# Kernel optimization log

Measured on AMD Instinct MI355X. Metric: run time of the kernel, lower is better.

Reference implementation:

```python
import jax, jax.numpy as jnp
import numpy as np

B, C, H, W = 2, 192, 64, 64
NHEADS = 8


def setup_inputs() -> dict:
    key = jax.random.key(0)
    ks = jax.random.split(key, 6)
    L = H * W
    return {
        "x": jax.random.normal(ks[0], (B, C, H, W), dtype=jnp.float32),
        "mask": jax.random.normal(ks[1], (B, L, L), dtype=jnp.float32),
        "w_qkv": jax.random.normal(ks[2], (3 * C, C), dtype=jnp.float32) * (1.0 / np.sqrt(C)),
        "b_qkv": jax.random.normal(ks[3], (3 * C,), dtype=jnp.float32) * 0.02,
        "w_proj": jax.random.normal(ks[4], (C, C), dtype=jnp.float32) * (1.0 / np.sqrt(C)),
        "b_proj": jax.random.normal(ks[5], (C,), dtype=jnp.float32) * 0.02,
        "num_heads": NHEADS,
    }


def reference(x, mask, w_qkv, b_qkv, w_proj, b_proj, num_heads):
    b, c, h, w = x.shape
    L = h * w
    hd = c // num_heads  # head dim
    # 1x1 conv == per-pixel linear over channels
    qkv = jnp.einsum('bchw,oc->bohw', x, w_qkv) + b_qkv[None, :, None, None]
    q, k, v = jnp.split(qkv, 3, axis=1)  # each [b, c, h, w]

    def to_heads(t):
        # b (head hd) h w -> b head (h w) hd
        return t.reshape(b, num_heads, hd, L).transpose(0, 1, 3, 2)

    q, k, v = to_heads(q), to_heads(k), to_heads(v)
    scale = num_heads ** (-0.5)  # NOTE: original scales by num_heads, not head_dim
    attn = jnp.einsum('bnld,bnmd->bnlm', q, k) * scale + mask[:, None, :, :]
    attn = jax.nn.softmax(attn, axis=-1)
    out = jnp.einsum('bnlm,bnmd->bnld', attn, v)  # [b, head, L, hd]
    # b head L hd -> b (head hd) h w
    out = out.transpose(0, 1, 3, 2).reshape(b, c, h, w)
    out = jnp.einsum('bchw,oc->bohw', out, w_proj) + b_proj[None, :, None, None]
    return out
```

## Files before the change

### kernel.cpp

```cpp
#include <hip/hip_runtime.h>

#define B_  2
#define C_  192
#define L_  4096
#define NH_ 8
#define HD_ 24
#define C3_ 576
#define KV_ 64
#define NSPL_ 4
#define LSPL_ (L_ / NSPL_)
#define NTS_ (LSPL_ / KV_)
#define HG_ 4
#define KSTR_ 20

typedef _Float16 f16;
typedef __attribute__((ext_vector_type(8))) f16 f16x8;
typedef __attribute__((ext_vector_type(16))) float f32x16;

#define L2E_ 1.4426950408889634f

__device__ __forceinline__ int pk2(float a, float b) {
    union { __fp16 h __attribute__((ext_vector_type(2))); int i; } u;
    u.h = __builtin_amdgcn_cvt_pkrtz(a, b);
    return u.i;
}
__device__ __forceinline__ int pk2_rte(float a, float b) {
    union { f16 h[2]; int i; } u;
    u.h[0] = (f16)a; u.h[1] = (f16)b;
    return u.i;
}
__device__ __forceinline__ float ex2(float x) {
    float r;
    asm("v_exp_f32 %0, %1" : "=v"(r) : "v"(x));
    return r;
}
__device__ __forceinline__ float lg2(float x) {
    float r;
    asm("v_log_f32 %0, %1" : "=v"(r) : "v"(x));
    return r;
}

union Frag { f16x8 v; int i[4]; };

#define MFMA32(A, Bx, Cc) __builtin_amdgcn_mfma_f32_32x32x16_f16((A), (Bx), (Cc), 0, 0, 0)

__device__ __forceinline__ void gload4(const void* g, void* lds) {
    typedef const unsigned int __attribute__((address_space(1))) as1u;
    typedef unsigned int __attribute__((address_space(3))) as3u;
    __builtin_amdgcn_global_load_lds((as1u*)g,
                                     (as3u*)(unsigned int)(unsigned long long)lds,
                                     4, 0, 0);
}
__device__ __forceinline__ void gload16(const void* g, void* lds) {
    typedef const unsigned int __attribute__((address_space(1))) as1u;
    typedef unsigned int __attribute__((address_space(3))) as3u;
    __builtin_amdgcn_global_load_lds((as1u*)g,
                                     (as3u*)(unsigned int)(unsigned long long)lds,
                                     16, 0, 0);
}

__global__ __launch_bounds__(256) void lin_qkv(const float* __restrict__ a,
                                               const float* __restrict__ w,
                                               const float* __restrict__ bias,
                                               unsigned int* __restrict__ q2,
                                               unsigned int* __restrict__ k2t,
                                               unsigned short* __restrict__ v16) {
    __shared__ float wl[8][C_];
    const int og  = blockIdx.x;
    const int b   = blockIdx.y >> 4;
    const int lt  = blockIdx.y & 15;
    const int tid = threadIdx.x;

    for (int e = tid; e < 8 * C_; e += 256) wl[e / C_][e % C_] = w[og * 8 * C_ + e];
    __syncthreads();

    const int l = lt * 256 + tid;
    float acc[8];
#pragma unroll
    for (int j = 0; j < 8; ++j) acc[j] = bias[og * 8 + j];

    const float* ap = a + (size_t)b * C_ * L_ + l;
#pragma unroll 2
    for (int c = 0; c < C_; ++c) {
        const float xv = ap[(size_t)c * L_];
#pragma unroll
        for (int j = 0; j < 8; ++j) acc[j] = fmaf(wl[j][c], xv, acc[j]);
    }

    const float qscale = 0.35355339059327373f * L2E_;
    if (og < 24) {
        const int h = og / 3, j0 = (og % 3) * 4;
        unsigned int* p = q2 + ((size_t)(b * NH_ + h) * 12 + j0) * L_ + l;
#pragma unroll
        for (int j = 0; j < 4; ++j)
            p[(size_t)j * L_] = pk2_rte(acc[2 * j] * qscale, acc[2 * j + 1] * qscale);
    } else if (og < 48) {
        const int og_ = og - 24;
        const int h = og_ / 3, j0 = (og_ % 3) * 4;
        unsigned int* p = k2t + ((size_t)(b * NH_ + h) * L_ + l) * KSTR_ + j0;
        int4 v;
        v.x = pk2_rte(acc[0], acc[1]); v.y = pk2_rte(acc[2], acc[3]);
        v.z = pk2_rte(acc[4], acc[5]); v.w = pk2_rte(acc[6], acc[7]);
        *(int4*)p = v;
        if (j0 == 8) {
            int4 z; z.x = z.y = z.z = z.w = 0;
            *(int4*)(p + 4) = z;
            *(int4*)(p + 8) = z;
        }
    } else {
        const int og_ = og - 48;
        const int h = og_ / 3, d0 = (og_ % 3) * 8;
        unsigned short* p = v16 + ((size_t)(b * NH_ + h) * 24 + d0) * L_ + l;
#pragma unroll
        for (int j = 0; j < 8; ++j) {
            union { f16 hf; unsigned short us; } cv;
            cv.hf = (f16)acc[j];
            p[(size_t)j * L_] = cv.us;
        }
    }
}

__global__ __launch_bounds__(256) void lin_kernel(const float* __restrict__ a,
                                                  const float* __restrict__ w,
                                                  const float* __restrict__ bias,
                                                  float* __restrict__ out, int OC) {
    __shared__ float wl[8][C_];
    const int og  = blockIdx.x;
    const int b   = blockIdx.y >> 4;
    const int lt  = blockIdx.y & 15;
    const int tid = threadIdx.x;

    for (int e = tid; e < 8 * C_; e += 256) wl[e / C_][e % C_] = w[og * 8 * C_ + e];
    __syncthreads();

    const int l = lt * 256 + tid;
    float acc[8];
#pragma unroll
    for (int j = 0; j < 8; ++j) acc[j] = bias[og * 8 + j];

    const float* ap = a + (size_t)b * C_ * L_ + l;
#pragma unroll 2
    for (int c = 0; c < C_; ++c) {
        const float xv = ap[(size_t)c * L_];
#pragma unroll
        for (int j = 0; j < 8; ++j) acc[j] = fmaf(wl[j][c], xv, acc[j]);
    }

    float* op = out + ((size_t)b * OC + og * 8) * L_ + l;
#pragma unroll
    for (int j = 0; j < 8; ++j) op[(size_t)j * L_] = acc[j];
}

__global__ __launch_bounds__(256) void attn_mfma(const unsigned int* __restrict__ q2,
                                                 const unsigned int* __restrict__ k2t,
                                                 const unsigned short* __restrict__ v16,
                                                 const float* __restrict__ mask,
                                                 unsigned short* __restrict__ po,
                                                 float* __restrict__ pms) {
    const int tid  = threadIdx.x;
    const int lane = tid & 63;
    const int wid  = tid >> 6;
    const int hi   = lane >> 5;
    const int lq   = lane & 31;
    const int bid  = blockIdx.x;
    const int qt   = bid & 31;
    const int r    = bid >> 5;
    const int b    = r & 1;
    const int hg   = (r >> 1) & 1;
    const int sp   = r >> 2;
    const int qrow = qt * 128 + wid * 32 + lq;
    const int kv0  = sp * LSPL_;
    const int hbase = hg * HG_;

    __shared__ __attribute__((aligned(16))) int k_lds[2][HG_][64 * KSTR_];
    __shared__ __attribute__((aligned(16))) int v_lds[2][HG_][32 * 32];

    const unsigned int*   qb   = q2  + (size_t)(b * NH_ + hbase) * 12 * L_;
    const unsigned int*   kb_w = k2t + (size_t)(b * NH_ + hbase + wid) * L_ * KSTR_;
    const unsigned short* vb_w = v16 + (size_t)(b * NH_ + hbase + wid) * 24 * L_;
    const float* mrow = mask + ((size_t)b * L_ + qrow) * L_;

    int bq[HG_][8];
#pragma unroll
    for (int H = 0; H < HG_; ++H)
#pragma unroll
        for (int s = 0; s < 2; ++s)
#pragma unroll
            for (int t = 0; t < 4; ++t) {
                const int dpq = 8 * s + 4 * hi + t;
                bq[H][s * 4 + t] = (dpq < 12) ? qb[(size_t)(H * 12 + dpq) * L_ + qrow] : 0;
            }

#define STAGE(BF, KK) do {                                                    \
    const char* ksrc_ = (const char*)kb_w + (size_t)(KK) * 80 + (size_t)lane * 16; \
    char* kdst_ = (char*)&k_lds[BF][wid][0];                                  \
    _Pragma("unroll")                                                         \
    for (int j_ = 0; j_ < 5; ++j_)                                            \
        gload16(ksrc_ + j_ * 1024, kdst_ + j_ * 1024);                        \
    _Pragma("unroll")                                                         \
    for (int j_ = 0; j_ < 12; ++j_) {                                         \
        const int d_ = j_ * 2 + (lane >> 5);                                  \
        const int c_ = lane & 31;                                             \
        const int kp_ = ((((c_ >> 2) ^ (d_ & 7)) << 2) | (c_ & 3));           \
        gload4(vb_w + (size_t)d_ * L_ + (KK) + 2 * kp_,                       \
               (char*)&v_lds[BF][wid][0] + j_ * 256);                         \
    } } while (0)

#define MLOADX(KK) do {                                                       \
    const float4* mb_ = (const float4*)(mrow + (KK));                         \
    _Pragma("unroll")                                                         \
    for (int q_ = 0; q_ < 4; ++q_) {                                          \
        const float4 t0_ = mb_[2 * q_ + hi];                                  \
        mr0[4 * q_ + 0] = t0_.x; mr0[4 * q_ + 1] = t0_.y;                     \
        mr0[4 * q_ + 2] = t0_.z; mr0[4 * q_ + 3] = t0_.w;                     \
        const float4 t1_ = mb_[8 + 2 * q_ + hi];                              \
        mr1[4 * q_ + 0] = t1_.x; mr1[4 * q_ + 1] = t1_.y;                     \
        mr1[4 * q_ + 2] = t1_.z; mr1[4 * q_ + 3] = t1_.w;                     \
    } } while (0)

#define MSCALE do {                                                           \
    _Pragma("unroll")                                                         \
    for (int i_ = 0; i_ < 16; ++i_) { mr0[i_] *= L2E_; mr1[i_] *= L2E_; }     \
    } while (0)

#define QKH(BF, H, C0, C1) do {                                               \
    Frag qf0, qf1, ka;                                                        \
    _Pragma("unroll")                                                         \
    for (int t_ = 0; t_ < 4; ++t_) { qf0.i[t_] = bq[H][t_]; qf1.i[t_] = bq[H][4 + t_]; } \
    const int* kb_ = &k_lds[BF][H][0];                                        \
    ka.v = *(const f16x8*)(kb_ + lq * KSTR_ + 4 * hi);                        \
    C0 = MFMA32(ka.v, qf0.v, mr0);                                            \
    ka.v = *(const f16x8*)(kb_ + lq * KSTR_ + 8 + 4 * hi);                    \
    C0 = MFMA32(ka.v, qf1.v, C0);                                             \
    ka.v = *(const f16x8*)(kb_ + (32 + lq) * KSTR_ + 4 * hi);                 \
    C1 = MFMA32(ka.v, qf0.v, mr1);                                            \
    ka.v = *(const f16x8*)(kb_ + (32 + lq) * KSTR_ + 8 + 4 * hi);             \
    C1 = MFMA32(ka.v, qf1.v, C1);                                             \
    } while (0)

#define SMH(H, C0, C1) do {                                                   \
    float m8[8], m4[4], m2[2];                                                \
    _Pragma("unroll")                                                         \
    for (int i_ = 0; i_ < 8; ++i_)                                            \
        m8[i_] = fmaxf(fmaxf(C0[i_], C0[i_ + 8]), fmaxf(C1[i_], C1[i_ + 8])); \
    _Pragma("unroll")                                                         \
    for (int i_ = 0; i_ < 4; ++i_) m4[i_] = fmaxf(m8[i_], m8[i_ + 4]);        \
    m2[0] = fmaxf(m4[0], m4[2]); m2[1] = fmaxf(m4[1], m4[3]);                 \
    float pmax = fmaxf(m2[0], m2[1]);                                         \
    pmax = fmaxf(pmax, __shfl_xor(pmax, 32));                                 \
    const float newm_ = fmaxf(mrun[H], pmax);                                 \
    const float r_ = ex2(mrun[H] - newm_);                                    \
    mrun[H] = newm_;                                                          \
    srun[H] *= r_;                                                            \
    _Pragma("unroll")                                                         \
    for (int i_ = 0; i_ < 16; ++i_) o[H][i_] *= r_;                           \
    _Pragma("unroll")                                                         \
    for (int i_ = 0; i_ < 16; ++i_) C0[i_] = ex2(C0[i_] - newm_);             \
    _Pragma("unroll")                                                         \
    for (int i_ = 0; i_ < 16; ++i_) C1[i_] = ex2(C1[i_] - newm_);             \
    float s8[8], s4[4];                                                       \
    _Pragma("unroll")                                                         \
    for (int i_ = 0; i_ < 8; ++i_)                                            \
        s8[i_] = (C0[i_] + C0[i_ + 8]) + (C1[i_] + C1[i_ + 8]);               \
    _Pragma("unroll")                                                         \
    for (int i_ = 0; i_ < 4; ++i_) s4[i_] = s8[i_] + s8[i_ + 4];              \
    float ls = (s4[0] + s4[2]) + (s4[1] + s4[3]);                             \
    ls += __shfl_xor(ls, 32);                                                 \
    srun[H] += ls;                                                            \
    } while (0)

#define PVH(BF, H, C0, C1) do {                                               \
    int wa1[4], wa2[4], sa1[4], sa2[4];                                       \
    int wb1[4], wb2[4], sb1[4], sb2[4];                                       \
    _Pragma("unroll")                                                         \
    for (int q_ = 0; q_ < 4; ++q_) {                                          \
        wa1[q_] = pk2(C0[4 * q_], C0[4 * q_ + 1]);                            \
        wa2[q_] = pk2(C0[4 * q_ + 2], C0[4 * q_ + 3]);                        \
        wb1[q_] = pk2(C1[4 * q_], C1[4 * q_ + 1]);                            \
        wb2[q_] = pk2(C1[4 * q_ + 2], C1[4 * q_ + 3]);                        \
    }                                                                         \
    _Pragma("unroll")                                                         \
    for (int q_ = 0; q_ < 4; ++q_) {                                          \
        sa1[q_] = __shfl_xor(wa1[q_], 32); sa2[q_] = __shfl_xor(wa2[q_], 32); \
        sb1[q_] = __shfl_xor(wb1[q_], 32); sb2[q_] = __shfl_xor(wb2[q_], 32); \
    }                                                                         \
    const int* vb_ = &v_lds[BF][H][0];                                        \
    _Pragma("unroll")                                                         \
    for (int s_ = 0; s_ < 2; ++s_) {                                          \
        const int qq_ = 2 * s_ + hi;                                          \
        Frag pb, va;                                                          \
        pb.i[0] = hi ? sa1[qq_] : wa1[qq_];                                   \
        pb.i[1] = hi ? sa2[qq_] : wa2[qq_];                                   \
        pb.i[2] = hi ? wa1[qq_] : sa1[qq_];                                   \
        pb.i[3] = hi ? wa2[qq_] : sa2[qq_];                                   \
        va.v = *(const f16x8*)(vb_ + lq * 32 + (((2 * s_ + hi) ^ (lq & 7)) << 2)); \
        o[H] = MFMA32(va.v, pb.v, o[H]);                                      \
        pb.i[0] = hi ? sb1[qq_] : wb1[qq_];                                   \
        pb.i[1] = hi ? sb2[qq_] : wb2[qq_];                                   \
        pb.i[2] = hi ? wb1[qq_] : sb1[qq_];                                   \
        pb.i[3] = hi ? wb2[qq_] : sb2[qq_];                                   \
        va.v = *(const f16x8*)(vb_ + lq * 32 + (((4 + 2 * s_ + hi) ^ (lq & 7)) << 2)); \
        o[H] = MFMA32(va.v, pb.v, o[H]);                                      \
    } } while (0)

    f32x16 o[HG_];
    float mrun[HG_], srun[HG_];
#pragma unroll
    for (int H = 0; H < HG_; ++H) {
#pragma unroll
        for (int i = 0; i < 16; ++i) o[H][i] = 0.f;
        mrun[H] = -1e30f;
        srun[H] = 0.f;
    }
    f32x16 mr0, mr1, cA0, cA1, cB0, cB1;

    STAGE(0, kv0);
    MLOADX(kv0);
    __syncthreads();

#pragma clang loop unroll(disable)
    for (int t = 0; t < NTS_; ++t) {
        const int kk = kv0 + t * KV_;
        const int cur = t & 1;
        if (t + 1 < NTS_) STAGE(cur ^ 1, kk + KV_);
        MSCALE;
        QKH(cur, 0, cA0, cA1);
        QKH(cur, 1, cB0, cB1);
        SMH(0, cA0, cA1);
        SMH(1, cB0, cB1);
        PVH(cur, 0, cA0, cA1);
        PVH(cur, 1, cB0, cB1);
        QKH(cur, 2, cA0, cA1);
        QKH(cur, 3, cB0, cB1);
        if (t + 1 < NTS_) MLOADX(kk + KV_);
        SMH(2, cA0, cA1);
        SMH(3, cB0, cB1);
        PVH(cur, 2, cA0, cA1);
        PVH(cur, 3, cB0, cB1);
        __syncthreads();
    }

#pragma unroll
    for (int H = 0; H < HG_; ++H) {
        const float inv = 1.f / srun[H];
        const float lse = mrun[H] + lg2(srun[H]);
        unsigned short* pob = po + ((size_t)((sp * B_ + b) * NH_ + hbase + H) * HD_) * L_ + qrow;
#pragma unroll
        for (int i = 0; i < 16; ++i) {
            const int d = (i & 3) + 8 * (i >> 2) + 4 * hi;
            if (d < HD_) {
                union { __fp16 hf; unsigned short us; } cv;
                cv.hf = (__fp16)(o[H][i] * inv);
                pob[(size_t)d * L_] = cv.us;
            }
        }
        if (hi == 0)
            pms[((size_t)(sp * B_ + b) * NH_ + hbase + H) * L_ + qrow] = lse;
    }
#undef STAGE
#undef MLOADX
#undef MSCALE
#undef QKH
#undef SMH
#undef PVH
}

__global__ __launch_bounds__(256) void combine_kernel(const unsigned short* __restrict__ po,
                                                      const float* __restrict__ pms,
                                                      float* __restrict__ att) {
    const int qrow = blockIdx.x * 256 + threadIdx.x;
    const int h    = blockIdx.y;
    const int b    = blockIdx.z;

    float l[NSPL_];
#pragma unroll
    for (int s = 0; s < NSPL_; ++s)
        l[s] = pms[((size_t)(s * B_ + b) * NH_ + h) * L_ + qrow];
    float lm = l[0];
#pragma unroll
    for (int s = 1; s < NSPL_; ++s) lm = fmaxf(lm, l[s]);
    float wv[NSPL_], wsum = 0.f;
#pragma unroll
    for (int s = 0; s < NSPL_; ++s) { wv[s] = ex2(l[s] - lm); wsum += wv[s]; }
    const float inv = 1.f / wsum;

    float* op = att + ((size_t)b * C_ + h * HD_) * L_ + qrow;
#pragma unroll
    for (int d = 0; d < HD_; ++d) {
        float acc = 0.f;
#pragma unroll
        for (int s = 0; s < NSPL_; ++s) {
            union { unsigned short us; __fp16 hf; } cv;
            cv.us = po[(((size_t)(s * B_ + b) * NH_ + h) * HD_ + d) * L_ + qrow];
            acc += (float)cv.hf * wv[s];
        }
        op[(size_t)d * L_] = acc * inv;
    }
}

extern "C" void kernel_launch(void* const* d_in, const int* in_sizes, int n_in,
                              void* d_out, int out_size, void* d_ws, size_t ws_size,
                              hipStream_t stream) {
    const float* x      = (const float*)d_in[0];
    const float* mask   = (const float*)d_in[1];
    const float* w_qkv  = (const float*)d_in[2];
    const float* b_qkv  = (const float*)d_in[3];
    const float* w_proj = (const float*)d_in[4];
    const float* b_proj = (const float*)d_in[5];
    float* out = (float*)d_out;

    unsigned int*   q2  = (unsigned int*)d_ws;
    unsigned int*   k2t = q2 + (size_t)B_ * NH_ * 12 * L_;
    unsigned short* v16 = (unsigned short*)(k2t + (size_t)B_ * NH_ * L_ * KSTR_);
    unsigned short* po  = v16 + (size_t)B_ * NH_ * HD_ * L_;
    float* pms    = (float*)(po + (size_t)NSPL_ * B_ * NH_ * HD_ * L_);
    float* ws_att = pms + (size_t)NSPL_ * B_ * NH_ * L_;

    lin_qkv<<<dim3(72, 32), 256, 0, stream>>>(x, w_qkv, b_qkv, q2, k2t, v16);
    attn_mfma<<<dim3(512), 256, 0, stream>>>(q2, k2t, v16, mask, po, pms);
    combine_kernel<<<dim3(16, NH_, B_), 256, 0, stream>>>(po, pms, ws_att);
    lin_kernel<<<dim3(24, 32), 256, 0, stream>>>(ws_att, w_proj, b_proj, out, C_);
}
```

Measured before the change: 354.0 us.

## Read K/V straight from global memory and double-buffer mask tiles in registers

```diff
diff --git a/kernel.cpp b/kernel.cpp
--- a/kernel.cpp
+++ b/kernel.cpp
@@ -43,21 +43,6 @@
 union Frag { f16x8 v; int i[4]; };
 
 #define MFMA32(A, Bx, Cc) __builtin_amdgcn_mfma_f32_32x32x16_f16((A), (Bx), (Cc), 0, 0, 0)
-
-__device__ __forceinline__ void gload4(const void* g, void* lds) {
-    typedef const unsigned int __attribute__((address_space(1))) as1u;
-    typedef unsigned int __attribute__((address_space(3))) as3u;
-    __builtin_amdgcn_global_load_lds((as1u*)g,
-                                     (as3u*)(unsigned int)(unsigned long long)lds,
-                                     4, 0, 0);
-}
-__device__ __forceinline__ void gload16(const void* g, void* lds) {
-    typedef const unsigned int __attribute__((address_space(1))) as1u;
-    typedef unsigned int __attribute__((address_space(3))) as3u;
-    __builtin_amdgcn_global_load_lds((as1u*)g,
-                                     (as3u*)(unsigned int)(unsigned long long)lds,
-                                     16, 0, 0);
-}
 
 __global__ __launch_bounds__(256) void lin_qkv(const float* __restrict__ a,
                                                const float* __restrict__ w,
@@ -110,7 +95,7 @@
     } else {
         const int og_ = og - 48;
         const int h = og_ / 3, d0 = (og_ % 3) * 8;
-        unsigned short* p = v16 + ((size_t)(b * NH_ + h) * 24 + d0) * L_ + l;
+        unsigned short* p = v16 + ((size_t)(b * NH_ + h) * 32 + d0) * L_ + l;
 #pragma unroll
         for (int j = 0; j < 8; ++j) {
             union { f16 hf; unsigned short us; } cv;
@@ -172,12 +157,9 @@
     const int kv0  = sp * LSPL_;
     const int hbase = hg * HG_;
 
-    __shared__ __attribute__((aligned(16))) int k_lds[2][HG_][64 * KSTR_];
-    __shared__ __attribute__((aligned(16))) int v_lds[2][HG_][32 * 32];
-
-    const unsigned int*   qb   = q2  + (size_t)(b * NH_ + hbase) * 12 * L_;
-    const unsigned int*   kb_w = k2t + (size_t)(b * NH_ + hbase + wid) * L_ * KSTR_;
-    const unsigned short* vb_w = v16 + (size_t)(b * NH_ + hbase + wid) * 24 * L_;
+    const unsigned int*   qb  = q2  + (size_t)(b * NH_ + hbase) * 12 * L_;
+    const int*            kb0 = (const int*)k2t + (size_t)(b * NH_ + hbase) * L_ * KSTR_;
+    const unsigned short* vb0 = v16 + (size_t)(b * NH_ + hbase) * 32 * L_;
     const float* mrow = mask + ((size_t)b * L_ + qrow) * L_;
 
     int bq[HG_][8];
@@ -191,50 +173,26 @@
                 bq[H][s * 4 + t] = (dpq < 12) ? qb[(size_t)(H * 12 + dpq) * L_ + qrow] : 0;
             }
 
-#define STAGE(BF, KK) do {                                                    \
-    const char* ksrc_ = (const char*)kb_w + (size_t)(KK) * 80 + (size_t)lane * 16; \
-    char* kdst_ = (char*)&k_lds[BF][wid][0];                                  \
-    _Pragma("unroll")                                                         \
-    for (int j_ = 0; j_ < 5; ++j_)                                            \
-        gload16(ksrc_ + j_ * 1024, kdst_ + j_ * 1024);                        \
-    _Pragma("unroll")                                                         \
-    for (int j_ = 0; j_ < 12; ++j_) {                                         \
-        const int d_ = j_ * 2 + (lane >> 5);                                  \
-        const int c_ = lane & 31;                                             \
-        const int kp_ = ((((c_ >> 2) ^ (d_ & 7)) << 2) | (c_ & 3));           \
-        gload4(vb_w + (size_t)d_ * L_ + (KK) + 2 * kp_,                       \
-               (char*)&v_lds[BF][wid][0] + j_ * 256);                         \
+#define MLOADX(MD, KK) do {                                                   \
+    const float4* mb_ = (const float4*)(mrow + (KK));                         \
+    _Pragma("unroll")                                                         \
+    for (int q_ = 0; q_ < 4; ++q_) {                                          \
+        MD[q_]     = mb_[2 * q_ + hi];                                        \
+        MD[4 + q_] = mb_[8 + 2 * q_ + hi];                                    \
     } } while (0)
 
-#define MLOADX(KK) do {                                                       \
-    const float4* mb_ = (const float4*)(mrow + (KK));                         \
-    _Pragma("unroll")                                                         \
-    for (int q_ = 0; q_ < 4; ++q_) {                                          \
-        const float4 t0_ = mb_[2 * q_ + hi];                                  \
-        mr0[4 * q_ + 0] = t0_.x; mr0[4 * q_ + 1] = t0_.y;                     \
-        mr0[4 * q_ + 2] = t0_.z; mr0[4 * q_ + 3] = t0_.w;                     \
-        const float4 t1_ = mb_[8 + 2 * q_ + hi];                              \
-        mr1[4 * q_ + 0] = t1_.x; mr1[4 * q_ + 1] = t1_.y;                     \
-        mr1[4 * q_ + 2] = t1_.z; mr1[4 * q_ + 3] = t1_.w;                     \
-    } } while (0)
-
-#define MSCALE do {                                                           \
-    _Pragma("unroll")                                                         \
-    for (int i_ = 0; i_ < 16; ++i_) { mr0[i_] *= L2E_; mr1[i_] *= L2E_; }     \
-    } while (0)
-
-#define QKH(BF, H, C0, C1) do {                                               \
+#define QKH(H, KK, C0, C1) do {                                               \
     Frag qf0, qf1, ka;                                                        \
     _Pragma("unroll")                                                         \
     for (int t_ = 0; t_ < 4; ++t_) { qf0.i[t_] = bq[H][t_]; qf1.i[t_] = bq[H][4 + t_]; } \
-    const int* kb_ = &k_lds[BF][H][0];                                        \
-    ka.v = *(const f16x8*)(kb_ + lq * KSTR_ + 4 * hi);                        \
+    const int* kb_ = kb0 + (size_t)(H) * L_ * KSTR_;                          \
+    ka.v = *(const f16x8*)(kb_ + (size_t)((KK) + lq) * KSTR_ + 4 * hi);       \
     C0 = MFMA32(ka.v, qf0.v, mr0);                                            \
-    ka.v = *(const f16x8*)(kb_ + lq * KSTR_ + 8 + 4 * hi);                    \
+    ka.v = *(const f16x8*)(kb_ + (size_t)((KK) + lq) * KSTR_ + 8 + 4 * hi);   \
     C0 = MFMA32(ka.v, qf1.v, C0);                                             \
-    ka.v = *(const f16x8*)(kb_ + (32 + lq) * KSTR_ + 4 * hi);                 \
+    ka.v = *(const f16x8*)(kb_ + (size_t)((KK) + 32 + lq) * KSTR_ + 4 * hi);  \
     C1 = MFMA32(ka.v, qf0.v, mr1);                                            \
-    ka.v = *(const f16x8*)(kb_ + (32 + lq) * KSTR_ + 8 + 4 * hi);             \
+    ka.v = *(const f16x8*)(kb_ + (size_t)((KK) + 32 + lq) * KSTR_ + 8 + 4 * hi); \
     C1 = MFMA32(ka.v, qf1.v, C1);                                             \
     } while (0)
 
@@ -269,7 +227,7 @@
     srun[H] += ls;                                                            \
     } while (0)
 
-#define PVH(BF, H, C0, C1) do {                                               \
+#define PVH(H, KK, C0, C1) do {                                               \
     int wa1[4], wa2[4], sa1[4], sa2[4];                                       \
     int wb1[4], wb2[4], sb1[4], sb2[4];                                       \
     _Pragma("unroll")                                                         \
@@ -284,7 +242,7 @@
         sa1[q_] = __shfl_xor(wa1[q_], 32); sa2[q_] = __shfl_xor(wa2[q_], 32); \
         sb1[q_] = __shfl_xor(wb1[q_], 32); sb2[q_] = __shfl_xor(wb2[q_], 32); \
     }                                                                         \
-    const int* vb_ = &v_lds[BF][H][0];                                        \
+    const unsigned short* vb_ = vb0 + (size_t)(H) * 32 * L_ + (size_t)lq * L_ + (KK) + 8 * hi; \
     _Pragma("unroll")                                                         \
     for (int s_ = 0; s_ < 2; ++s_) {                                          \
         const int qq_ = 2 * s_ + hi;                                          \
@@ -293,15 +251,39 @@
         pb.i[1] = hi ? sa2[qq_] : wa2[qq_];                                   \
         pb.i[2] = hi ? wa1[qq_] : sa1[qq_];                                   \
         pb.i[3] = hi ? wa2[qq_] : sa2[qq_];                                   \
-        va.v = *(const f16x8*)(vb_ + lq * 32 + (((2 * s_ + hi) ^ (lq & 7)) << 2)); \
+        va.v = *(const f16x8*)(vb_ + 16 * s_);                                \
         o[H] = MFMA32(va.v, pb.v, o[H]);                                      \
         pb.i[0] = hi ? sb1[qq_] : wb1[qq_];                                   \
         pb.i[1] = hi ? sb2[qq_] : wb2[qq_];                                   \
         pb.i[2] = hi ? wb1[qq_] : sb1[qq_];                                   \
         pb.i[3] = hi ? wb2[qq_] : sb2[qq_];                                   \
-        va.v = *(const f16x8*)(vb_ + lq * 32 + (((4 + 2 * s_ + hi) ^ (lq & 7)) << 2)); \
+        va.v = *(const f16x8*)(vb_ + 32 + 16 * s_);                           \
         o[H] = MFMA32(va.v, pb.v, o[H]);                                      \
     } } while (0)
+
+#define COMPUTE(KK, MC) do {                                                  \
+    f32x16 mr0, mr1;                                                          \
+    _Pragma("unroll")                                                         \
+    for (int q_ = 0; q_ < 4; ++q_) {                                          \
+        mr0[4 * q_ + 0] = MC[q_].x * L2E_; mr0[4 * q_ + 1] = MC[q_].y * L2E_; \
+        mr0[4 * q_ + 2] = MC[q_].z * L2E_; mr0[4 * q_ + 3] = MC[q_].w * L2E_; \
+        mr1[4 * q_ + 0] = MC[4 + q_].x * L2E_; mr1[4 * q_ + 1] = MC[4 + q_].y * L2E_; \
+        mr1[4 * q_ + 2] = MC[4 + q_].z * L2E_; mr1[4 * q_ + 3] = MC[4 + q_].w * L2E_; \
+    }                                                                         \
+    f32x16 cA0, cA1, cB0, cB1;                                                \
+    QKH(0, KK, cA0, cA1);                                                     \
+    QKH(1, KK, cB0, cB1);                                                     \
+    SMH(0, cA0, cA1);                                                         \
+    SMH(1, cB0, cB1);                                                         \
+    PVH(0, KK, cA0, cA1);                                                     \
+    PVH(1, KK, cB0, cB1);                                                     \
+    QKH(2, KK, cA0, cA1);                                                     \
+    QKH(3, KK, cB0, cB1);                                                     \
+    SMH(2, cA0, cA1);                                                         \
+    SMH(3, cB0, cB1);                                                         \
+    PVH(2, KK, cA0, cA1);                                                     \
+    PVH(3, KK, cB0, cB1);                                                     \
+    } while (0)
 
     f32x16 o[HG_];
     float mrun[HG_], srun[HG_];
@@ -312,32 +294,17 @@
         mrun[H] = -1e30f;
         srun[H] = 0.f;
     }
-    f32x16 mr0, mr1, cA0, cA1, cB0, cB1;
-
-    STAGE(0, kv0);
-    MLOADX(kv0);
-    __syncthreads();
+    float4 mc[8], mn[8];
+
+    MLOADX(mc, kv0);
 
 #pragma clang loop unroll(disable)
-    for (int t = 0; t < NTS_; ++t) {
+    for (int t = 0; t < NTS_; t += 2) {
         const int kk = kv0 + t * KV_;
-        const int cur = t & 1;
-        if (t + 1 < NTS_) STAGE(cur ^ 1, kk + KV_);
-        MSCALE;
-        QKH(cur, 0, cA0, cA1);
-        QKH(cur, 1, cB0, cB1);
-        SMH(0, cA0, cA1);
-        SMH(1, cB0, cB1);
-        PVH(cur, 0, cA0, cA1);
-        PVH(cur, 1, cB0, cB1);
-        QKH(cur, 2, cA0, cA1);
-        QKH(cur, 3, cB0, cB1);
-        if (t + 1 < NTS_) MLOADX(kk + KV_);
-        SMH(2, cA0, cA1);
-        SMH(3, cB0, cB1);
-        PVH(cur, 2, cA0, cA1);
-        PVH(cur, 3, cB0, cB1);
-        __syncthreads();
+        MLOADX(mn, kk + KV_);
+        COMPUTE(kk, mc);
+        if (t + 2 < NTS_) MLOADX(mc, kk + 2 * KV_);
+        COMPUTE(kk + KV_, mn);
     }
 
 #pragma unroll
@@ -357,12 +324,11 @@
         if (hi == 0)
             pms[((size_t)(sp * B_ + b) * NH_ + hbase + H) * L_ + qrow] = lse;
     }
-#undef STAGE
 #undef MLOADX
-#undef MSCALE
 #undef QKH
 #undef SMH
 #undef PVH
+#undef COMPUTE
 }
 
 __global__ __launch_bounds__(256) void combine_kernel(const unsigned short* __restrict__ po,
@@ -412,7 +378,7 @@
     unsigned int*   q2  = (unsigned int*)d_ws;
     unsigned int*   k2t = q2 + (size_t)B_ * NH_ * 12 * L_;
     unsigned short* v16 = (unsigned short*)(k2t + (size_t)B_ * NH_ * L_ * KSTR_);
-    unsigned short* po  = v16 + (size_t)B_ * NH_ * HD_ * L_;
+    unsigned short* po  = v16 + (size_t)B_ * NH_ * 32 * L_;
     float* pms    = (float*)(po + (size_t)NSPL_ * B_ * NH_ * HD_ * L_);
     float* ws_att = pms + (size_t)NSPL_ * B_ * NH_ * L_;
 
```

After: 366.7 us. 1.04x slower.
